# Optimization experiments

Measured on AMD Instinct MI355X. Metric: run time of the kernel, lower is better.

The kernel has to match this reference:

```python
import jax, jax.numpy as jnp
import numpy as np

LEAK = 0.2

def setup_inputs() -> dict:
    key = jax.random.key(0)
    ks = jax.random.split(key, 8)
    B, D, H1, H2, F = 2048, 3072, 512, 256, 100
    s = lambda fan_in: 1.0 / np.sqrt(fan_in)
    return {
        "x":  jax.random.normal(ks[0], (B, D), dtype=jnp.float32),
        "W1": jax.random.uniform(ks[1], (D, H1), jnp.float32, -s(D), s(D)),
        "b1": jnp.zeros((H1,), jnp.float32),
        "W2": jax.random.uniform(ks[2], (H1, H2), jnp.float32, -s(H1), s(H1)),
        "b2": jnp.zeros((H2,), jnp.float32),
        "T":  jax.random.normal(ks[3], (H2, F), dtype=jnp.float32),
        "Wf": jax.random.uniform(ks[4], (H2 + F, 1), jnp.float32, -s(H2 + F), s(H2 + F)),
        "bf": jnp.zeros((1,), jnp.float32),
    }

def reference(x, W1, b1, W2, b2, T, Wf, bf):
    # MLP stack with LeakyReLU(0.2)
    h = jax.nn.leaky_relu(x @ W1 + b1, LEAK)          # (B,512)
    h = jax.nn.leaky_relu(h @ W2 + b2, LEAK)          # (B,256)
    # Minibatch discrimination: pairwise L1 per feature, exp, sum over batch
    m = h @ T                                          # (B,100)
    d = jnp.abs(m[:, None, :] - m[None, :, :])         # (B,B,100)
    feats = jnp.sum(jnp.exp(-d), axis=1)               # (B,100)
    z = jnp.concatenate([h, feats], axis=1)            # (B,356)
    return z @ Wf + bf                                 # (B,1)
```

## Files before the change

kernel.cpp:

```cpp
#include <hip/hip_runtime.h>
#include <hip/hip_bf16.h>

#define LEAK 0.2f

typedef __attribute__((ext_vector_type(8))) short short8;
typedef __attribute__((ext_vector_type(4))) float f32x4;

union bfpack { int4 i; __hip_bfloat16 h[8]; };

__device__ __forceinline__ void transpose_tile(float (*tile)[33], int t,
                                               const float* __restrict__ W,
                                               __hip_bfloat16* __restrict__ Wt,
                                               int K, int N, int kblk, int nblk) {
  int k0 = kblk * 32, n0 = nblk * 32;
  int tx = t & 31, ty = t >> 5;
#pragma unroll
  for (int r = 0; r < 4; ++r) {
    int n = n0 + tx;
    tile[ty + r * 8][tx] = (n < N) ? W[(long)(k0 + ty + r * 8) * N + n] : 0.f;
  }
  __syncthreads();
#pragma unroll
  for (int r = 0; r < 4; ++r)
    Wt[(long)(n0 + ty + r * 8) * K + k0 + tx] = __float2bfloat16(tile[tx][ty + r * 8]);
}

__global__ __launch_bounds__(256) void k_prep(const float* __restrict__ W1,
                                              __hip_bfloat16* __restrict__ W1t) {
  __shared__ float tile[32][33];
  int b = blockIdx.x;
  transpose_tile(tile, threadIdx.x, W1, W1t, 3072, 512, b % 96, b / 96);
}

__global__ __launch_bounds__(256) void k_gemm1(const float* __restrict__ A,
                                               const __hip_bfloat16* __restrict__ Bt,
                                               float* __restrict__ Cp,
                                               const float* __restrict__ W2,
                                               __hip_bfloat16* __restrict__ W2t,
                                               const float* __restrict__ T,
                                               __hip_bfloat16* __restrict__ Tt) {
  const int K = 3072, N = 512, KSPL = 1024;
  __shared__ __align__(16) __hip_bfloat16 As[64][72];
  __shared__ __align__(16) __hip_bfloat16 Bs[64][72];
  int gid = blockIdx.x;
  int tid = threadIdx.x;
  if (gid >= 768) {
    float (*tile)[33] = (float(*)[33])&As[0][0];
    int b = gid - 768;
    if (b < 128) transpose_tile(tile, tid, W2, W2t, 512, 256, b % 16, b / 16);
    else { b -= 128; transpose_tile(tile, tid, T, Tt, 256, 100, b % 8, b / 8); }
    return;
  }
  int mt = gid & 31, nt = (gid >> 5) & 7, z = gid >> 8;
  int lane = tid & 63, wv = tid >> 6;
  int wm = wv & 1, wn = wv >> 1, quad = lane >> 4, l16 = lane & 15;
  long m0 = (long)mt * 64, n0 = (long)nt * 64;
  int kStart = z * KSPL;
  int srow = tid >> 2, scol = (tid & 3) * 16;
  const float* Ag = A + (m0 + srow) * K + kStart + scol;
  const __hip_bfloat16* Bg = Bt + (n0 + srow) * K + kStart + scol;

  auto loadA = [&](int kb, int4& o0, int4& o1) {
    float4 f0 = *reinterpret_cast<const float4*>(Ag + kb);
    float4 f1 = *reinterpret_cast<const float4*>(Ag + kb + 4);
    float4 f2 = *reinterpret_cast<const float4*>(Ag + kb + 8);
    float4 f3 = *reinterpret_cast<const float4*>(Ag + kb + 12);
    bfpack u0, u1;
    u0.h[0] = __float2bfloat16(f0.x); u0.h[1] = __float2bfloat16(f0.y);
    u0.h[2] = __float2bfloat16(f0.z); u0.h[3] = __float2bfloat16(f0.w);
    u0.h[4] = __float2bfloat16(f1.x); u0.h[5] = __float2bfloat16(f1.y);
    u0.h[6] = __float2bfloat16(f1.z); u0.h[7] = __float2bfloat16(f1.w);
    u1.h[0] = __float2bfloat16(f2.x); u1.h[1] = __float2bfloat16(f2.y);
    u1.h[2] = __float2bfloat16(f2.z); u1.h[3] = __float2bfloat16(f2.w);
    u1.h[4] = __float2bfloat16(f3.x); u1.h[5] = __float2bfloat16(f3.y);
    u1.h[6] = __float2bfloat16(f3.z); u1.h[7] = __float2bfloat16(f3.w);
    o0 = u0.i; o1 = u1.i;
  };

  int4 ra0, ra1, rb0, rb1;
  loadA(0, ra0, ra1);
  rb0 = *reinterpret_cast<const int4*>(Bg);
  rb1 = *reinterpret_cast<const int4*>(Bg + 8);

  f32x4 acc[2][2] = {};
  for (int kb = 0; kb < KSPL; kb += 64) {
    *reinterpret_cast<int4*>(&As[srow][scol]) = ra0;
    *reinterpret_cast<int4*>(&As[srow][scol + 8]) = ra1;
    *reinterpret_cast<int4*>(&Bs[srow][scol]) = rb0;
    *reinterpret_cast<int4*>(&Bs[srow][scol + 8]) = rb1;
    __syncthreads();
    if (kb + 64 < KSPL) {
      loadA(kb + 64, ra0, ra1);
      rb0 = *reinterpret_cast<const int4*>(Bg + kb + 64);
      rb1 = *reinterpret_cast<const int4*>(Bg + kb + 72);
    }
#pragma unroll
    for (int half = 0; half < 2; ++half) {
      short8 af[2], bfr[2];
#pragma unroll
      for (int u = 0; u < 2; ++u) {
        af[u]  = *reinterpret_cast<const short8*>(&As[wm * 32 + u * 16 + l16][half * 32 + quad * 8]);
        bfr[u] = *reinterpret_cast<const short8*>(&Bs[wn * 32 + u * 16 + l16][half * 32 + quad * 8]);
      }
#pragma unroll
      for (int tm = 0; tm < 2; ++tm)
#pragma unroll
        for (int tn = 0; tn < 2; ++tn)
          acc[tm][tn] =
              __builtin_amdgcn_mfma_f32_16x16x32_bf16(af[tm], bfr[tn], acc[tm][tn], 0, 0, 0);
    }
    __syncthreads();
  }

  float* Cz = Cp + (long)z * 2048 * 512;
#pragma unroll
  for (int tm = 0; tm < 2; ++tm)
#pragma unroll
    for (int tn = 0; tn < 2; ++tn)
#pragma unroll
      for (int r = 0; r < 4; ++r) {
        long gm = m0 + wm * 32 + tm * 16 + quad * 4 + r;
        long gn = n0 + wn * 32 + tn * 16 + l16;
        Cz[gm * N + gn] = acc[tm][tn][r];
      }
}

__global__ __launch_bounds__(256) void k_gemm2(const float* __restrict__ P1,
                                               const float* __restrict__ b1,
                                               const __hip_bfloat16* __restrict__ Bt,
                                               const float* __restrict__ b2,
                                               __hip_bfloat16* __restrict__ h2b,
                                               float* __restrict__ h2f) {
  const int K = 512, N = 256;
  const long FS = 2048L * 512;
  __shared__ __align__(16) __hip_bfloat16 As[64][72];
  __shared__ __align__(16) __hip_bfloat16 Bs[64][72];
  int tid = threadIdx.x, lane = tid & 63, wv = tid >> 6;
  int wm = wv & 1, wn = wv >> 1, quad = lane >> 4, l16 = lane & 15;
  long m0 = (long)blockIdx.x * 64, n0 = (long)blockIdx.y * 64;
  int srow = tid >> 2, scol = (tid & 3) * 16;
  const float* Ag = P1 + (m0 + srow) * K + scol;
  const __hip_bfloat16* Bg = Bt + (n0 + srow) * K + scol;

  auto loadA = [&](int kb, int4& o0, int4& o1) {
    float4 v[4];
#pragma unroll
    for (int j = 0; j < 4; ++j) v[j] = *reinterpret_cast<const float4*>(Ag + kb + j * 4);
#pragma unroll
    for (int z = 1; z < 3; ++z)
#pragma unroll
      for (int j = 0; j < 4; ++j) {
        float4 a = *reinterpret_cast<const float4*>(Ag + z * FS + kb + j * 4);
        v[j].x += a.x; v[j].y += a.y; v[j].z += a.z; v[j].w += a.w;
      }
#pragma unroll
    for (int j = 0; j < 4; ++j) {
      float4 bs = *reinterpret_cast<const float4*>(b1 + kb + scol + j * 4);
      v[j].x += bs.x; v[j].y += bs.y; v[j].z += bs.z; v[j].w += bs.w;
      v[j].x = v[j].x > 0.f ? v[j].x : LEAK * v[j].x;
      v[j].y = v[j].y > 0.f ? v[j].y : LEAK * v[j].y;
      v[j].z = v[j].z > 0.f ? v[j].z : LEAK * v[j].z;
      v[j].w = v[j].w > 0.f ? v[j].w : LEAK * v[j].w;
    }
    bfpack u0, u1;
    u0.h[0] = __float2bfloat16(v[0].x); u0.h[1] = __float2bfloat16(v[0].y);
    u0.h[2] = __float2bfloat16(v[0].z); u0.h[3] = __float2bfloat16(v[0].w);
    u0.h[4] = __float2bfloat16(v[1].x); u0.h[5] = __float2bfloat16(v[1].y);
    u0.h[6] = __float2bfloat16(v[1].z); u0.h[7] = __float2bfloat16(v[1].w);
    u1.h[0] = __float2bfloat16(v[2].x); u1.h[1] = __float2bfloat16(v[2].y);
    u1.h[2] = __float2bfloat16(v[2].z); u1.h[3] = __float2bfloat16(v[2].w);
    u1.h[4] = __float2bfloat16(v[3].x); u1.h[5] = __float2bfloat16(v[3].y);
    u1.h[6] = __float2bfloat16(v[3].z); u1.h[7] = __float2bfloat16(v[3].w);
    o0 = u0.i; o1 = u1.i;
  };

  int4 ra0, ra1, rb0, rb1;
  loadA(0, ra0, ra1);
  rb0 = *reinterpret_cast<const int4*>(Bg);
  rb1 = *reinterpret_cast<const int4*>(Bg + 8);

  f32x4 acc[2][2] = {};
  for (int kb = 0; kb < K; kb += 64) {
    *reinterpret_cast<int4*>(&As[srow][scol]) = ra0;
    *reinterpret_cast<int4*>(&As[srow][scol + 8]) = ra1;
    *reinterpret_cast<int4*>(&Bs[srow][scol]) = rb0;
    *reinterpret_cast<int4*>(&Bs[srow][scol + 8]) = rb1;
    __syncthreads();
    if (kb + 64 < K) {
      loadA(kb + 64, ra0, ra1);
      rb0 = *reinterpret_cast<const int4*>(Bg + kb + 64);
      rb1 = *reinterpret_cast<const int4*>(Bg + kb + 72);
    }
#pragma unroll
    for (int half = 0; half < 2; ++half) {
      short8 af[2], bfr[2];
#pragma unroll
      for (int u = 0; u < 2; ++u) {
        af[u]  = *reinterpret_cast<const short8*>(&As[wm * 32 + u * 16 + l16][half * 32 + quad * 8]);
        bfr[u] = *reinterpret_cast<const short8*>(&Bs[wn * 32 + u * 16 + l16][half * 32 + quad * 8]);
      }
#pragma unroll
      for (int tm = 0; tm < 2; ++tm)
#pragma unroll
        for (int tn = 0; tn < 2; ++tn)
          acc[tm][tn] =
              __builtin_amdgcn_mfma_f32_16x16x32_bf16(af[tm], bfr[tn], acc[tm][tn], 0, 0, 0);
    }
    __syncthreads();
  }

#pragma unroll
  for (int tm = 0; tm < 2; ++tm)
#pragma unroll
    for (int tn = 0; tn < 2; ++tn)
#pragma unroll
      for (int r = 0; r < 4; ++r) {
        long gm = m0 + wm * 32 + tm * 16 + quad * 4 + r;
        long gn = n0 + wn * 32 + tn * 16 + l16;
        float v = acc[tm][tn][r] + b2[gn];
        v = v > 0.f ? v : LEAK * v;
        h2b[gm * N + gn] = __float2bfloat16(v);
        h2f[gm * N + gn] = v;
      }
}

__global__ __launch_bounds__(256) void k_gemm3(const __hip_bfloat16* __restrict__ A,
                                               const __hip_bfloat16* __restrict__ Bt,
                                               float* __restrict__ Cp) {
  const int K = 256;
  __shared__ __align__(16) __hip_bfloat16 As[64][72];
  __shared__ __align__(16) __hip_bfloat16 Bs[64][72];
  int tid = threadIdx.x;
  int lane = tid & 63, wv = tid >> 6;
  int wm = wv & 1, wn = wv >> 1, quad = lane >> 4, l16 = lane & 15;
  long m0 = (long)blockIdx.x * 64, n0 = (long)blockIdx.y * 64;
  int kStart = blockIdx.z * 64;
  int srow = tid >> 2, scol = (tid & 3) * 16;
  const __hip_bfloat16* Ag = A + (m0 + srow) * K + kStart + scol;
  const __hip_bfloat16* Bg = Bt + (n0 + srow) * K + kStart + scol;

  *reinterpret_cast<int4*>(&As[srow][scol]) = *reinterpret_cast<const int4*>(Ag);
  *reinterpret_cast<int4*>(&As[srow][scol + 8]) = *reinterpret_cast<const int4*>(Ag + 8);
  *reinterpret_cast<int4*>(&Bs[srow][scol]) = *reinterpret_cast<const int4*>(Bg);
  *reinterpret_cast<int4*>(&Bs[srow][scol + 8]) = *reinterpret_cast<const int4*>(Bg + 8);
  __syncthreads();
  f32x4 acc[2][2] = {};
#pragma unroll
  for (int half = 0; half < 2; ++half) {
    short8 af[2], bfr[2];
#pragma unroll
    for (int u = 0; u < 2; ++u) {
      af[u]  = *reinterpret_cast<const short8*>(&As[wm * 32 + u * 16 + l16][half * 32 + quad * 8]);
      bfr[u] = *reinterpret_cast<const short8*>(&Bs[wn * 32 + u * 16 + l16][half * 32 + quad * 8]);
    }
#pragma unroll
    for (int tm = 0; tm < 2; ++tm)
#pragma unroll
      for (int tn = 0; tn < 2; ++tn)
        acc[tm][tn] =
            __builtin_amdgcn_mfma_f32_16x16x32_bf16(af[tm], bfr[tn], acc[tm][tn], 0, 0, 0);
  }
  float* Cz = Cp + (long)blockIdx.z * 2048 * 128;
#pragma unroll
  for (int tm = 0; tm < 2; ++tm)
#pragma unroll
    for (int tn = 0; tn < 2; ++tn)
#pragma unroll
      for (int r = 0; r < 4; ++r) {
        long gm = m0 + wm * 32 + tm * 16 + quad * 4 + r;
        long gn = n0 + wn * 32 + tn * 16 + l16;
        Cz[gn * 2048 + gm] = acc[tm][tn][r];
      }
}

__global__ __launch_bounds__(1024) void k_bucketfeats(const float* __restrict__ mTz,
                                                      float* __restrict__ featsT) {
  __shared__ float sP[2048], sN[2048];
  __shared__ float Sp[2048], Sn[2048];
  __shared__ int Smeta[2048];
  __shared__ short sB[2048];
  __shared__ int cnt[256], bstart[256], bcur[256];
  __shared__ float bsP[256], bsN[256], Pbel[256], Nab[256];
  __shared__ float wred[32];
  __shared__ float sMin, sMax;
  int f = blockIdx.x;
  int t = threadIdx.x;
  int lane = t & 63, wv = t >> 6;
  const long FS = 2048L * 128;
  const float* row = mTz + (long)f * 2048;

  float m[2];
  float lmin = 3.4e38f, lmax = -3.4e38f;
#pragma unroll
  for (int r = 0; r < 2; ++r) {
    int e = t + r * 1024;
    float v = row[e] + row[FS + e] + row[2 * FS + e] + row[3 * FS + e];
    m[r] = v;
    lmin = fminf(lmin, v);
    lmax = fmaxf(lmax, v);
  }
#pragma unroll
  for (int d = 32; d; d >>= 1) {
    lmin = fminf(lmin, __shfl_down(lmin, d));
    lmax = fmaxf(lmax, __shfl_down(lmax, d));
  }
  if (lane == 0) { wred[wv] = lmin; wred[16 + wv] = lmax; }
  if (t < 256) cnt[t] = 0;
  __syncthreads();
  if (t == 0) {
    float a = wred[0], b = wred[16];
    for (int i = 1; i < 16; ++i) { a = fminf(a, wred[i]); b = fmaxf(b, wred[16 + i]); }
    sMin = a; sMax = b;
  }
  __syncthreads();
  float mn = sMin, mx = sMax;
  float rge = mx - mn;
  float scale = (rge > 1e-20f) ? 255.0f / rge : 0.f;
  float mid = 0.5f * (mn + mx);
#pragma unroll
  for (int r = 0; r < 2; ++r) {
    int e = t + r * 1024;
    float v = m[r];
    int b = (int)((v - mn) * scale);
    b = b < 255 ? b : 255;
    float arg = fminf(fmaxf(v - mid, -60.f), 60.f);
    sP[e] = __expf(arg);
    sN[e] = __expf(-arg);
    sB[e] = (short)b;
    atomicAdd(&cnt[b], 1);
  }
  __syncthreads();
  if (wv == 0) {
    int b4 = lane * 4;
    int c0 = cnt[b4], c1 = cnt[b4 + 1], c2 = cnt[b4 + 2], c3 = cnt[b4 + 3];
    int tot = c0 + c1 + c2 + c3;
    int inc = tot;
#pragma unroll
    for (int d = 1; d < 64; d <<= 1) {
      int y = __shfl_up(inc, d);
      if (lane >= d) inc += y;
    }
    int run = inc - tot;
    bstart[b4] = run; bcur[b4] = run; run += c0;
    bstart[b4 + 1] = run; bcur[b4 + 1] = run; run += c1;
    bstart[b4 + 2] = run; bcur[b4 + 2] = run; run += c2;
    bstart[b4 + 3] = run; bcur[b4 + 3] = run;
  }
  __syncthreads();
#pragma unroll
  for (int r = 0; r < 2; ++r) {
    int e = t + r * 1024;
    int b = sB[e];
    int slot = atomicAdd(&bcur[b], 1);
    Sp[slot] = sP[e];
    Sn[slot] = sN[e];
    Smeta[slot] = (b << 16) | e;
  }
  __syncthreads();
  if (t < 256) {
    int s0 = bstart[t], s1 = s0 + cnt[t];
    float ap = 0.f, an = 0.f;
    for (int q = s0; q < s1; ++q) { ap += Sp[q]; an += Sn[q]; }
    bsP[t] = ap; bsN[t] = an;
  }
  __syncthreads();
  if (wv == 0) {
    int b4 = lane * 4;
    float p0 = bsP[b4], p1 = bsP[b4 + 1], p2 = bsP[b4 + 2], p3 = bsP[b4 + 3];
    float n0 = bsN[b4], n1 = bsN[b4 + 1], n2 = bsN[b4 + 2], n3 = bsN[b4 + 3];
    float tp = p0 + p1 + p2 + p3, tn = n0 + n1 + n2 + n3;
    float ip = tp, in_ = tn;
#pragma unroll
    for (int d = 1; d < 64; d <<= 1) {
      float yp = __shfl_up(ip, d);
      float yn = __shfl_up(in_, d);
      if (lane >= d) { ip += yp; in_ += yn; }
    }
    float totn = __shfl(in_, 63);
    float runp = ip - tp;
    float runn = in_ - tn;
    Pbel[b4] = runp; Nab[b4] = totn - runn - n0; runp += p0; runn += n0;
    Pbel[b4 + 1] = runp; Nab[b4 + 1] = totn - runn - n1; runp += p1; runn += n1;
    Pbel[b4 + 2] = runp; Nab[b4 + 2] = totn - runn - n2; runp += p2; runn += n2;
    Pbel[b4 + 3] = runp; Nab[b4 + 3] = totn - runn - n3;
  }
  __syncthreads();
#pragma unroll
  for (int r = 0; r < 2; ++r) {
    int s = t + r * 1024;
    int meta = Smeta[s];
    int b = meta >> 16;
    int idx = meta & 0xFFFF;
    float p = Sp[s], n = Sn[s];
    float acc = n * Pbel[b] + p * Nab[b];
    int q0 = bstart[b], q1 = q0 + cnt[b];
    for (int q = q0; q < q1; ++q) acc += fminf(p * Sn[q], n * Sp[q]);
    featsT[(long)f * 2048 + idx] = acc;
  }
}

__global__ __launch_bounds__(256) void k_final(const float* __restrict__ h2f,
                                               const float* __restrict__ featsT,
                                               const float* __restrict__ Wf,
                                               const float* __restrict__ bfp,
                                               float* __restrict__ out) {
  int wv = threadIdx.x >> 6, lane = threadIdx.x & 63;
  long i = (long)blockIdx.x * 4 + wv;
  const float* hrow = h2f + i * 256;
  float s = 0.f;
#pragma unroll
  for (int c = lane; c < 256; c += 64) s += hrow[c] * Wf[c];
  for (int f = lane; f < 100; f += 64) s += featsT[(long)f * 2048 + i] * Wf[256 + f];
#pragma unroll
  for (int off = 32; off; off >>= 1) s += __shfl_down(s, off);
  if (lane == 0) out[i] = s + bfp[0];
}

extern "C" void kernel_launch(void* const* d_in, const int* in_sizes, int n_in,
                              void* d_out, int out_size, void* d_ws, size_t ws_size,
                              hipStream_t stream) {
  const float* x  = (const float*)d_in[0];
  const float* W1 = (const float*)d_in[1];
  const float* b1 = (const float*)d_in[2];
  const float* W2 = (const float*)d_in[3];
  const float* b2 = (const float*)d_in[4];
  const float* T  = (const float*)d_in[5];
  const float* Wf = (const float*)d_in[6];
  const float* bf = (const float*)d_in[7];
  float* out = (float*)d_out;

  char* w = (char*)d_ws;
  auto alloc = [&](size_t b) { char* p = w; w += (b + 255) & ~(size_t)255; return p; };
  __hip_bfloat16* W1t = (__hip_bfloat16*)alloc(512L * 3072 * 2);
  __hip_bfloat16* W2t = (__hip_bfloat16*)alloc(256L * 512 * 2);
  __hip_bfloat16* Tt  = (__hip_bfloat16*)alloc(128L * 256 * 2);
  float*          h2f = (float*)alloc(2048L * 256 * 4);
  __hip_bfloat16* h2b = (__hip_bfloat16*)alloc(2048L * 256 * 2);
  float*          feT = (float*)alloc(100L * 2048 * 4);
  float*          P1  = (float*)alloc(3L * 2048 * 512 * 4);
  float*          P3  = (float*)alloc(4L * 2048 * 128 * 4);

  k_prep<<<1536, 256, 0, stream>>>(W1, W1t);
  k_gemm1<<<928, 256, 0, stream>>>(x, W1t, P1, W2, W2t, T, Tt);
  k_gemm2<<<dim3(32, 4), 256, 0, stream>>>(P1, b1, W2t, b2, h2b, h2f);
  k_gemm3<<<dim3(32, 2, 4), 256, 0, stream>>>(h2b, Tt, P3);
  k_bucketfeats<<<100, 1024, 0, stream>>>(P3, feT);
  k_final<<<512, 256, 0, stream>>>(h2f, feT, Wf, bf, out);
}
```

Before: 136.7 us.

## Pre-convert x to bf16 in prep kernel and drop fp32 h2 buffer

New measurement: 132.5 us. 1.03x faster.

```diff
diff --git a/kernel.cpp b/kernel.cpp
--- a/kernel.cpp
+++ b/kernel.cpp
@@ -8,10 +8,50 @@
 
 union bfpack { int4 i; __hip_bfloat16 h[8]; };
 
-__device__ __forceinline__ void transpose_tile(float (*tile)[33], int t,
-                                               const float* __restrict__ W,
-                                               __hip_bfloat16* __restrict__ Wt,
-                                               int K, int N, int kblk, int nblk) {
+__device__ __forceinline__ float bf2f(unsigned short u) {
+  union { unsigned v; float f; } c;
+  c.v = ((unsigned)u) << 16;
+  return c.f;
+}
+
+__global__ __launch_bounds__(256) void k_prep(const float* __restrict__ x,
+                                              __hip_bfloat16* __restrict__ xb,
+                                              const float* __restrict__ W1,
+                                              __hip_bfloat16* __restrict__ W1t,
+                                              const float* __restrict__ W2,
+                                              __hip_bfloat16* __restrict__ W2t,
+                                              const float* __restrict__ T,
+                                              __hip_bfloat16* __restrict__ Tt) {
+  int b = blockIdx.x;
+  int t = threadIdx.x;
+  if (b < 6144) {
+    int idx = b * 256 + t;
+    float4 v = reinterpret_cast<const float4*>(x)[idx];
+    union { ushort4 u; __hip_bfloat16 h[4]; } c;
+    c.h[0] = __float2bfloat16(v.x);
+    c.h[1] = __float2bfloat16(v.y);
+    c.h[2] = __float2bfloat16(v.z);
+    c.h[3] = __float2bfloat16(v.w);
+    reinterpret_cast<ushort4*>(xb)[idx] = c.u;
+    return;
+  }
+  __shared__ float tile[32][33];
+  const float* W;
+  __hip_bfloat16* Wt;
+  int K, N, kblk, nblk;
+  int b2 = b - 6144;
+  if (b2 < 1536) {
+    W = W1; Wt = W1t; K = 3072; N = 512;
+    kblk = b2 % 96; nblk = b2 / 96;
+  } else if (b2 < 1664) {
+    int b3 = b2 - 1536;
+    W = W2; Wt = W2t; K = 512; N = 256;
+    kblk = b3 % 16; nblk = b3 / 16;
+  } else {
+    int b4 = b2 - 1664;
+    W = T; Wt = Tt; K = 256; N = 100;
+    kblk = b4 % 8; nblk = b4 / 8;
+  }
   int k0 = kblk * 32, n0 = nblk * 32;
   int tx = t & 31, ty = t >> 5;
 #pragma unroll
@@ -25,62 +65,24 @@
     Wt[(long)(n0 + ty + r * 8) * K + k0 + tx] = __float2bfloat16(tile[tx][ty + r * 8]);
 }
 
-__global__ __launch_bounds__(256) void k_prep(const float* __restrict__ W1,
-                                              __hip_bfloat16* __restrict__ W1t) {
-  __shared__ float tile[32][33];
-  int b = blockIdx.x;
-  transpose_tile(tile, threadIdx.x, W1, W1t, 3072, 512, b % 96, b / 96);
-}
-
-__global__ __launch_bounds__(256) void k_gemm1(const float* __restrict__ A,
+__global__ __launch_bounds__(256) void k_gemm1(const __hip_bfloat16* __restrict__ A,
                                                const __hip_bfloat16* __restrict__ Bt,
-                                               float* __restrict__ Cp,
-                                               const float* __restrict__ W2,
-                                               __hip_bfloat16* __restrict__ W2t,
-                                               const float* __restrict__ T,
-                                               __hip_bfloat16* __restrict__ Tt) {
+                                               float* __restrict__ Cp) {
   const int K = 3072, N = 512, KSPL = 1024;
   __shared__ __align__(16) __hip_bfloat16 As[64][72];
   __shared__ __align__(16) __hip_bfloat16 Bs[64][72];
-  int gid = blockIdx.x;
-  int tid = threadIdx.x;
-  if (gid >= 768) {
-    float (*tile)[33] = (float(*)[33])&As[0][0];
-    int b = gid - 768;
-    if (b < 128) transpose_tile(tile, tid, W2, W2t, 512, 256, b % 16, b / 16);
-    else { b -= 128; transpose_tile(tile, tid, T, Tt, 256, 100, b % 8, b / 8); }
-    return;
-  }
-  int mt = gid & 31, nt = (gid >> 5) & 7, z = gid >> 8;
-  int lane = tid & 63, wv = tid >> 6;
+  int tid = threadIdx.x, lane = tid & 63, wv = tid >> 6;
   int wm = wv & 1, wn = wv >> 1, quad = lane >> 4, l16 = lane & 15;
-  long m0 = (long)mt * 64, n0 = (long)nt * 64;
-  int kStart = z * KSPL;
+  long m0 = (long)blockIdx.x * 64, n0 = (long)blockIdx.y * 64;
+  int kStart = blockIdx.z * KSPL;
   int srow = tid >> 2, scol = (tid & 3) * 16;
-  const float* Ag = A + (m0 + srow) * K + kStart + scol;
+  const __hip_bfloat16* Ag = A + (m0 + srow) * K + kStart + scol;
   const __hip_bfloat16* Bg = Bt + (n0 + srow) * K + kStart + scol;
 
-  auto loadA = [&](int kb, int4& o0, int4& o1) {
-    float4 f0 = *reinterpret_cast<const float4*>(Ag + kb);
-    float4 f1 = *reinterpret_cast<const float4*>(Ag + kb + 4);
-    float4 f2 = *reinterpret_cast<const float4*>(Ag + kb + 8);
-    float4 f3 = *reinterpret_cast<const float4*>(Ag + kb + 12);
-    bfpack u0, u1;
-    u0.h[0] = __float2bfloat16(f0.x); u0.h[1] = __float2bfloat16(f0.y);
-    u0.h[2] = __float2bfloat16(f0.z); u0.h[3] = __float2bfloat16(f0.w);
-    u0.h[4] = __float2bfloat16(f1.x); u0.h[5] = __float2bfloat16(f1.y);
-    u0.h[6] = __float2bfloat16(f1.z); u0.h[7] = __float2bfloat16(f1.w);
-    u1.h[0] = __float2bfloat16(f2.x); u1.h[1] = __float2bfloat16(f2.y);
-    u1.h[2] = __float2bfloat16(f2.z); u1.h[3] = __float2bfloat16(f2.w);
-    u1.h[4] = __float2bfloat16(f3.x); u1.h[5] = __float2bfloat16(f3.y);
-    u1.h[6] = __float2bfloat16(f3.z); u1.h[7] = __float2bfloat16(f3.w);
-    o0 = u0.i; o1 = u1.i;
-  };
-
-  int4 ra0, ra1, rb0, rb1;
-  loadA(0, ra0, ra1);
-  rb0 = *reinterpret_cast<const int4*>(Bg);
-  rb1 = *reinterpret_cast<const int4*>(Bg + 8);
+  int4 ra0 = *reinterpret_cast<const int4*>(Ag);
+  int4 ra1 = *reinterpret_cast<const int4*>(Ag + 8);
+  int4 rb0 = *reinterpret_cast<const int4*>(Bg);
+  int4 rb1 = *reinterpret_cast<const int4*>(Bg + 8);
 
   f32x4 acc[2][2] = {};
   for (int kb = 0; kb < KSPL; kb += 64) {
@@ -90,7 +92,8 @@
     *reinterpret_cast<int4*>(&Bs[srow][scol + 8]) = rb1;
     __syncthreads();
     if (kb + 64 < KSPL) {
-      loadA(kb + 64, ra0, ra1);
+      ra0 = *reinterpret_cast<const int4*>(Ag + kb + 64);
+      ra1 = *reinterpret_cast<const int4*>(Ag + kb + 72);
       rb0 = *reinterpret_cast<const int4*>(Bg + kb + 64);
       rb1 = *reinterpret_cast<const int4*>(Bg + kb + 72);
     }
@@ -112,7 +115,7 @@
     __syncthreads();
   }
 
-  float* Cz = Cp + (long)z * 2048 * 512;
+  float* Cz = Cp + (long)blockIdx.z * 2048 * 512;
 #pragma unroll
   for (int tm = 0; tm < 2; ++tm)
 #pragma unroll
@@ -129,8 +132,7 @@
                                                const float* __restrict__ b1,
                                                const __hip_bfloat16* __restrict__ Bt,
                                                const float* __restrict__ b2,
-                                               __hip_bfloat16* __restrict__ h2b,
-                                               float* __restrict__ h2f) {
+                                               __hip_bfloat16* __restrict__ h2b) {
   const int K = 512, N = 256;
   const long FS = 2048L * 512;
   __shared__ __align__(16) __hip_bfloat16 As[64][72];
@@ -220,7 +222,6 @@
         float v = acc[tm][tn][r] + b2[gn];
         v = v > 0.f ? v : LEAK * v;
         h2b[gm * N + gn] = __float2bfloat16(v);
-        h2f[gm * N + gn] = v;
       }
 }
 
@@ -399,17 +400,17 @@
   }
 }
 
-__global__ __launch_bounds__(256) void k_final(const float* __restrict__ h2f,
+__global__ __launch_bounds__(256) void k_final(const __hip_bfloat16* __restrict__ h2b,
                                                const float* __restrict__ featsT,
                                                const float* __restrict__ Wf,
                                                const float* __restrict__ bfp,
                                                float* __restrict__ out) {
   int wv = threadIdx.x >> 6, lane = threadIdx.x & 63;
   long i = (long)blockIdx.x * 4 + wv;
-  const float* hrow = h2f + i * 256;
+  const unsigned short* hrow = reinterpret_cast<const unsigned short*>(h2b) + i * 256;
   float s = 0.f;
 #pragma unroll
-  for (int c = lane; c < 256; c += 64) s += hrow[c] * Wf[c];
+  for (int c = lane; c < 256; c += 64) s += bf2f(hrow[c]) * Wf[c];
   for (int f = lane; f < 100; f += 64) s += featsT[(long)f * 2048 + i] * Wf[256 + f];
 #pragma unroll
   for (int off = 32; off; off >>= 1) s += __shfl_down(s, off);
@@ -431,19 +432,19 @@
 
   char* w = (char*)d_ws;
   auto alloc = [&](size_t b) { char* p = w; w += (b + 255) & ~(size_t)255; return p; };
+  __hip_bfloat16* xb  = (__hip_bfloat16*)alloc(2048L * 3072 * 2);
   __hip_bfloat16* W1t = (__hip_bfloat16*)alloc(512L * 3072 * 2);
   __hip_bfloat16* W2t = (__hip_bfloat16*)alloc(256L * 512 * 2);
   __hip_bfloat16* Tt  = (__hip_bfloat16*)alloc(128L * 256 * 2);
-  float*          h2f = (float*)alloc(2048L * 256 * 4);
   __hip_bfloat16* h2b = (__hip_bfloat16*)alloc(2048L * 256 * 2);
   float*          feT = (float*)alloc(100L * 2048 * 4);
   float*          P1  = (float*)alloc(3L * 2048 * 512 * 4);
   float*          P3  = (float*)alloc(4L * 2048 * 128 * 4);
 
-  k_prep<<<1536, 256, 0, stream>>>(W1, W1t);
-  k_gemm1<<<928, 256, 0, stream>>>(x, W1t, P1, W2, W2t, T, Tt);
-  k_gemm2<<<dim3(32, 4), 256, 0, stream>>>(P1, b1, W2t, b2, h2b, h2f);
+  k_prep<<<7840, 256, 0, stream>>>(x, xb, W1, W1t, W2, W2t, T, Tt);
+  k_gemm1<<<dim3(32, 8, 3), 256, 0, stream>>>(xb, W1t, P1);
+  k_gemm2<<<dim3(32, 4), 256, 0, stream>>>(P1, b1, W2t, b2, h2b);
   k_gemm3<<<dim3(32, 2, 4), 256, 0, stream>>>(h2b, Tt, P3);
   k_bucketfeats<<<100, 1024, 0, stream>>>(P3, feT);
-  k_final<<<512, 256, 0, stream>>>(h2f, feT, Wf, bf, out);
-}
+  k_final<<<512, 256, 0, stream>>>(h2b, feT, Wf, bf, out);
+}
```
